# Kernel tuning notes

Hardware: AMD Instinct MI355X
Metric: run time of the kernel (lower is better)

The kernel has to match this reference:

```python
import jax, jax.numpy as jnp
import numpy as np

K = 1024
HEADS = 16


def setup_inputs() -> dict:
    key = jax.random.key(0)
    ks = jax.random.split(key, 6)
    x = jax.random.normal(ks[0], (2, 2048, K), dtype=jnp.float32)
    sc = 1.0 / np.sqrt(K)
    Wq = jax.random.normal(ks[1], (K, K), dtype=jnp.float32) * sc
    Wk = jax.random.normal(ks[2], (K, K), dtype=jnp.float32) * sc
    Wv = jax.random.normal(ks[3], (K, K), dtype=jnp.float32) * sc
    Wu = jax.random.normal(ks[4], (K, K), dtype=jnp.float32) * sc
    bu = jax.random.normal(ks[5], (K,), dtype=jnp.float32) * 0.01
    return {"x": x, "Wq": Wq, "Wk": Wk, "Wv": Wv, "Wu": Wu, "bu": bu}


def reference(x, Wq, Wk, Wv, Wu, bu):
    b, t, k = x.shape
    h = HEADS
    s = k // h
    # torch Linear: y = x @ W.T
    q = (x @ Wq.T).reshape(b, t, h, s)
    kk = (x @ Wk.T).reshape(b, t, h, s)
    v = (x @ Wv.T).reshape(b, t, h, s)
    # NOTE: original scales by sqrt(k) (full model dim), not sqrt(head dim)
    dot = jnp.einsum('bqhs,bkhs->bhqk', q, kk) / jnp.sqrt(jnp.float32(k))
    attn = jax.nn.softmax(dot, axis=-1)
    out = jnp.einsum('bhqk,bkhs->bqhs', attn, v).reshape(b, t, k)
    return out @ Wu.T + bu
```

## Files before the change

kernel.cpp:

```cpp
#include <hip/hip_runtime.h>
#include <hip/hip_bf16.h>


typedef __bf16 bf16x8 __attribute__((ext_vector_type(8)));
typedef float f32x4 __attribute__((ext_vector_type(4)));
typedef float f32x16 __attribute__((ext_vector_type(16)));
typedef unsigned int u32x4 __attribute__((ext_vector_type(4)));

static __device__ __forceinline__ unsigned short f2bf(float f) {
  union { float f; unsigned u; } a; a.f = f;
  unsigned r = a.u + 0x7fff + ((a.u >> 16) & 1);
  return (unsigned short)(r >> 16);
}

static __device__ __forceinline__ unsigned cvt_pk_bf16(float lo, float hi) {
  unsigned r;
  asm("v_cvt_pk_bf16_f32 %0, %1, %2" : "=v"(r) : "v"(lo), "v"(hi));
  return r;
}

static __device__ __forceinline__ float fexp2(float x) {
#if __has_builtin(__builtin_amdgcn_exp2f)
  return __builtin_amdgcn_exp2f(x);
#else
  float r; asm("v_exp_f32 %0, %1\n\ts_nop 0" : "=v"(r) : "v"(x)); return r;
#endif
}

static __device__ __forceinline__ void swap32(unsigned a, unsigned b,
                                              unsigned& x, unsigned& y, int hi) {
#if __has_builtin(__builtin_amdgcn_permlane32_swap)
  typedef unsigned u32x2 __attribute__((ext_vector_type(2)));
  u32x2 r = __builtin_amdgcn_permlane32_swap(a, b, false, false);
  x = r.x; y = r.y;
#else
  unsigned pa = (unsigned)__shfl_xor((int)a, 32, 64);
  unsigned pb = (unsigned)__shfl_xor((int)b, 32, 64);
  x = hi ? pb : a;
  y = hi ? b : pa;
#endif
}

static __device__ __forceinline__ void gload_lds16(const unsigned short* g, unsigned short* l) {
  __builtin_amdgcn_global_load_lds((const __attribute__((address_space(1))) void*)g,
                                   (__attribute__((address_space(3))) void*)l, 16, 0, 0);
}

static __device__ __forceinline__ float tsum16(const f32x16& v) {
  float a0 = v[0]+v[1], a1 = v[2]+v[3], a2 = v[4]+v[5], a3 = v[6]+v[7];
  float a4 = v[8]+v[9], a5 = v[10]+v[11], a6 = v[12]+v[13], a7 = v[14]+v[15];
  float b0 = a0+a1, b1 = a2+a3, b2 = a4+a5, b3 = a6+a7;
  return (b0+b1) + (b2+b3);
}

__global__ __launch_bounds__(256)
void cast_all(const float* __restrict__ x, const float* __restrict__ wq,
              const float* __restrict__ wk, const float* __restrict__ wv,
              const float* __restrict__ wu,
              unsigned short* __restrict__ xb, unsigned short* __restrict__ wqb,
              unsigned short* __restrict__ wkb, unsigned short* __restrict__ wvb,
              unsigned short* __restrict__ wub)
{
  int bid = blockIdx.x;
  const float* src; unsigned short* dst; int blk;
  if (bid < 4096)      { src = x;  dst = xb;  blk = bid; }
  else if (bid < 5120) { src = wq; dst = wqb; blk = bid - 4096; }
  else if (bid < 6144) { src = wk; dst = wkb; blk = bid - 5120; }
  else if (bid < 7168) { src = wv; dst = wvb; blk = bid - 6144; }
  else                 { src = wu; dst = wub; blk = bid - 7168; }
  int idx = blk * 1024 + threadIdx.x * 4;
  float4 v = *(const float4*)&src[idx];
  ushort4 o;
  o.x = f2bf(v.x); o.y = f2bf(v.y); o.z = f2bf(v.z); o.w = f2bf(v.w);
  *(ushort4*)&dst[idx] = o;
}

__global__ __launch_bounds__(512, 2)
void gemm_qkv(const unsigned short* __restrict__ A,
              const unsigned short* __restrict__ Bq,
              const unsigned short* __restrict__ Bk,
              const unsigned short* __restrict__ Bv,
              unsigned short* __restrict__ Qo,
              unsigned short* __restrict__ Ko,
              unsigned short* __restrict__ Vo)
{
  const int Ksz = 1024;
  __shared__ __align__(16) unsigned short As[2][128 * 64];
  __shared__ __align__(16) unsigned short Bs[2][128 * 64];
  const int z = blockIdx.z;
  const unsigned short* B = (z == 0) ? Bq : (z == 1) ? Bk : Bv;
  const int tid  = threadIdx.x;
  const int lane = tid & 63;
  const int wid  = tid >> 6;
  const int wr   = wid >> 2, wc = wid & 3;
  const int g    = lane >> 4, r = lane & 15;
  const int bm   = blockIdx.x * 128, bn = blockIdx.y * 128;

  f32x4 acc[4][2] = {};

  const int srow   = lane >> 3;
  const int schunk = (lane & 7) ^ srow;
  const unsigned short* Ag0 = &A[(size_t)(bm + wid*16 +     srow) * Ksz + schunk*8];
  const unsigned short* Ag1 = &A[(size_t)(bm + wid*16 + 8 + srow) * Ksz + schunk*8];
  const unsigned short* Bg0 = &B[(size_t)(bn + wid*16 +     srow) * Ksz + schunk*8];
  const unsigned short* Bg1 = &B[(size_t)(bn + wid*16 + 8 + srow) * Ksz + schunk*8];

  gload_lds16(Ag0, &As[0][(wid*16    ) * 64]);
  gload_lds16(Ag1, &As[0][(wid*16 + 8) * 64]);
  gload_lds16(Bg0, &Bs[0][(wid*16    ) * 64]);
  gload_lds16(Bg1, &Bs[0][(wid*16 + 8) * 64]);
  __syncthreads();

  int buf = 0;
  for (int k0 = 0; k0 < Ksz; k0 += 64) {
    if (k0 + 64 < Ksz) {
      gload_lds16(Ag0 + k0 + 64, &As[buf^1][(wid*16    ) * 64]);
      gload_lds16(Ag1 + k0 + 64, &As[buf^1][(wid*16 + 8) * 64]);
      gload_lds16(Bg0 + k0 + 64, &Bs[buf^1][(wid*16    ) * 64]);
      gload_lds16(Bg1 + k0 + 64, &Bs[buf^1][(wid*16 + 8) * 64]);
    }
#pragma unroll
    for (int kk = 0; kk < 2; ++kk) {
      bf16x8 af[4], bfr[2];
#pragma unroll
      for (int mi = 0; mi < 4; ++mi) {
        int row = wr*64 + mi*16 + r;
        int c = (g + kk*4) ^ (row & 7);
        af[mi] = *(const bf16x8*)&As[buf][row*64 + c*8];
      }
#pragma unroll
      for (int ni = 0; ni < 2; ++ni) {
        int row = wc*32 + ni*16 + r;
        int c = (g + kk*4) ^ (row & 7);
        bfr[ni] = *(const bf16x8*)&Bs[buf][row*64 + c*8];
      }
#pragma unroll
      for (int mi = 0; mi < 4; ++mi)
#pragma unroll
        for (int ni = 0; ni < 2; ++ni)
          acc[mi][ni] = __builtin_amdgcn_mfma_f32_16x16x32_bf16(af[mi], bfr[ni], acc[mi][ni], 0, 0, 0);
    }
    __syncthreads();
    buf ^= 1;
  }

  const float scale = (z == 0) ? (0.03125f * 1.4426950408889634f) : 1.0f;
#pragma unroll
  for (int mi = 0; mi < 4; ++mi)
#pragma unroll
    for (int ni = 0; ni < 2; ++ni) {
      if (z == 2) {
        int m0 = bm + wr*64 + mi*16 + g*4;
        int n  = bn + wc*32 + ni*16 + r;
        int b = m0 >> 11, t0 = m0 & 2047;
        int h = n >> 6,  s = n & 63;
        ushort4 o;
        o.x = f2bf(acc[mi][ni][0]); o.y = f2bf(acc[mi][ni][1]);
        o.z = f2bf(acc[mi][ni][2]); o.w = f2bf(acc[mi][ni][3]);
        *(ushort4*)&Vo[((size_t)((b*16 + h)*64 + s)) * 2048 + t0] = o;
      } else {
        unsigned short* dst = (z == 0) ? Qo : Ko;
#pragma unroll
        for (int q = 0; q < 4; ++q) {
          int m = bm + wr*64 + mi*16 + g*4 + q;
          int n = bn + wc*32 + ni*16 + r;
          int b = m >> 11, t = m & 2047;
          int h = n >> 6,  s = n & 63;
          dst[((size_t)((b*16 + h)*2048 + t)) * 64 + s] = f2bf(acc[mi][ni][q] * scale);
        }
      }
    }
}

__global__ __launch_bounds__(512, 2)
void gemm_final(const unsigned short* __restrict__ A,
                const unsigned short* __restrict__ B,
                float* __restrict__ Cf,
                const float* __restrict__ bias)
{
  const int Ksz = 1024, N = 1024;
  __shared__ __align__(16) unsigned short As[2][128 * 64];
  __shared__ __align__(16) unsigned short Bs[2][128 * 64];
  const int tid  = threadIdx.x;
  const int lane = tid & 63;
  const int wid  = tid >> 6;
  const int wr   = wid >> 2, wc = wid & 3;
  const int g    = lane >> 4, r = lane & 15;
  const int bm   = blockIdx.x * 128, bn = blockIdx.y * 128;

  f32x4 acc[4][2] = {};

  const int srow   = lane >> 3;
  const int schunk = (lane & 7) ^ srow;
  const unsigned short* Ag0 = &A[(size_t)(bm + wid*16 +     srow) * Ksz + schunk*8];
  const unsigned short* Ag1 = &A[(size_t)(bm + wid*16 + 8 + srow) * Ksz + schunk*8];
  const unsigned short* Bg0 = &B[(size_t)(bn + wid*16 +     srow) * Ksz + schunk*8];
  const unsigned short* Bg1 = &B[(size_t)(bn + wid*16 + 8 + srow) * Ksz + schunk*8];

  gload_lds16(Ag0, &As[0][(wid*16    ) * 64]);
  gload_lds16(Ag1, &As[0][(wid*16 + 8) * 64]);
  gload_lds16(Bg0, &Bs[0][(wid*16    ) * 64]);
  gload_lds16(Bg1, &Bs[0][(wid*16 + 8) * 64]);
  __syncthreads();

  int buf = 0;
  for (int k0 = 0; k0 < Ksz; k0 += 64) {
    if (k0 + 64 < Ksz) {
      gload_lds16(Ag0 + k0 + 64, &As[buf^1][(wid*16    ) * 64]);
      gload_lds16(Ag1 + k0 + 64, &As[buf^1][(wid*16 + 8) * 64]);
      gload_lds16(Bg0 + k0 + 64, &Bs[buf^1][(wid*16    ) * 64]);
      gload_lds16(Bg1 + k0 + 64, &Bs[buf^1][(wid*16 + 8) * 64]);
    }
#pragma unroll
    for (int kk = 0; kk < 2; ++kk) {
      bf16x8 af[4], bfr[2];
#pragma unroll
      for (int mi = 0; mi < 4; ++mi) {
        int row = wr*64 + mi*16 + r;
        int c = (g + kk*4) ^ (row & 7);
        af[mi] = *(const bf16x8*)&As[buf][row*64 + c*8];
      }
#pragma unroll
      for (int ni = 0; ni < 2; ++ni) {
        int row = wc*32 + ni*16 + r;
        int c = (g + kk*4) ^ (row & 7);
        bfr[ni] = *(const bf16x8*)&Bs[buf][row*64 + c*8];
      }
#pragma unroll
      for (int mi = 0; mi < 4; ++mi)
#pragma unroll
        for (int ni = 0; ni < 2; ++ni)
          acc[mi][ni] = __builtin_amdgcn_mfma_f32_16x16x32_bf16(af[mi], bfr[ni], acc[mi][ni], 0, 0, 0);
    }
    __syncthreads();
    buf ^= 1;
  }

#pragma unroll
  for (int mi = 0; mi < 4; ++mi)
#pragma unroll
    for (int ni = 0; ni < 2; ++ni)
#pragma unroll
      for (int q = 0; q < 4; ++q) {
        int m = bm + wr*64 + mi*16 + g*4 + q;
        int n = bn + wc*32 + ni*16 + r;
        Cf[(size_t)m * N + n] = acc[mi][ni][q] + bias[n];
      }
}

__global__ __launch_bounds__(256)
void attn_kernel(const unsigned short* __restrict__ Qg,
                 const unsigned short* __restrict__ Kg,
                 const unsigned short* __restrict__ Vtg,
                 unsigned short* __restrict__ Og)
{
  const int T = 2048;
  __shared__ __align__(16) unsigned short sK[2][128 * 64];
  __shared__ __align__(16) unsigned short sV[2][64 * 128];

  const int tid = threadIdx.x, lane = tid & 63, wid = tid >> 6;
  const int q32 = lane & 31;
  const int kh  = lane >> 5;

  int bid  = blockIdx.x + 16 * blockIdx.y;
  int nb   = (bid & 7) * 64 + (bid >> 3);
  int bh   = nb >> 4;
  int qblk = nb & 15;
  int qbase = qblk * 128 + wid * 32;

  const size_t base = (size_t)bh * T * 64;
  const unsigned short* Qh = Qg + base;
  const unsigned short* Kh = Kg + base;
  const unsigned short* Vh = Vtg + base;

  const int krow_l  = lane >> 3;
  const int kchunk  = (lane & 7) ^ (krow_l & 7);
  const int vrow_l  = lane >> 4;
  const int vchunkp = lane & 15;

  bf16x8 qf[4];
#pragma unroll
  for (int s = 0; s < 4; ++s)
    qf[s] = *(const bf16x8*)&Qh[(size_t)(qbase + q32)*64 + s*16 + kh*8];

  f32x16 oacc[2] = {};
  float l_own = 0.f;

#pragma unroll
  for (int r = 0; r < 4; ++r) {
    int kr = r*32 + wid*8;
    gload_lds16(Kh + (size_t)(kr + krow_l)*64 + kchunk*8, &sK[0][kr*64]);
    int vr = r*16 + wid*4;
    int vrow = vr + vrow_l;
    gload_lds16(Vh + (size_t)vrow*T + ((vchunkp ^ (vrow & 7))*8), &sV[0][vr*128]);
  }
  __syncthreads();

  int buf = 0;
#pragma unroll 1
  for (int t = 0; t < 16; ++t) {
    if (t < 15) {
      const int kv1 = (t + 1) * 128;
#pragma unroll
      for (int r = 0; r < 4; ++r) {
        int kr = r*32 + wid*8;
        gload_lds16(Kh + (size_t)(kv1 + kr + krow_l)*64 + kchunk*8,
                    &sK[buf^1][kr*64]);
        int vr = r*16 + wid*4;
        int vrow = vr + vrow_l;
        gload_lds16(Vh + (size_t)vrow*T + kv1 + ((vchunkp ^ (vrow & 7))*8),
                    &sV[buf^1][vr*128]);
      }
    }

#pragma unroll
    for (int st = 0; st < 4; ++st) {
      f32x16 a = {};
      const int kvr = st*32 + q32;
#pragma unroll
      for (int s = 0; s < 4; ++s) {
        const int c = (s*2 + kh) ^ (kvr & 7);
        bf16x8 kf = *(const bf16x8*)&sK[buf][kvr*64 + c*8];
        a = __builtin_amdgcn_mfma_f32_32x32x16_bf16(kf, qf[s], a, 0, 0, 0);
      }
#pragma unroll
      for (int r = 0; r < 16; ++r)
        a[r] = fexp2(a[r]);
      l_own += tsum16(a);

      unsigned U[8];
#pragma unroll
      for (int i = 0; i < 8; ++i)
        U[i] = cvt_pk_bf16(a[2*i], a[2*i + 1]);
      unsigned w[8];
      swap32(U[0], U[2], w[0], w[2], kh);
      swap32(U[1], U[3], w[1], w[3], kh);
      swap32(U[4], U[6], w[4], w[6], kh);
      swap32(U[5], U[7], w[5], w[7], kh);
#pragma unroll
      for (int c = 0; c < 2; ++c) {
        u32x4 pw = { w[c*4 + 0], w[c*4 + 1], w[c*4 + 2], w[c*4 + 3] };
        bf16x8 pf = __builtin_bit_cast(bf16x8, pw);
#pragma unroll
        for (int mt = 0; mt < 2; ++mt) {
          const int sr = mt*32 + q32;
          const int cc = (st*4 + c*2 + kh) ^ (sr & 7);
          bf16x8 vfr = *(const bf16x8*)&sV[buf][sr*128 + cc*8];
          oacc[mt] = __builtin_amdgcn_mfma_f32_32x32x16_bf16(vfr, pf, oacc[mt], 0, 0, 0);
        }
      }
    }

    __syncthreads();
    buf ^= 1;
  }

  const float l = l_own + __shfl_xor(l_own, 32, 64);
  const int h = bh & 15, b = bh >> 4;
  const float inv = 1.0f / l;
  const int tq = qbase + q32;
#pragma unroll
  for (int mt = 0; mt < 2; ++mt)
#pragma unroll
    for (int rg = 0; rg < 4; ++rg) {
      ushort4 o;
      o.x = f2bf(oacc[mt][rg*4 + 0] * inv);
      o.y = f2bf(oacc[mt][rg*4 + 1] * inv);
      o.z = f2bf(oacc[mt][rg*4 + 2] * inv);
      o.w = f2bf(oacc[mt][rg*4 + 3] * inv);
      int sd = mt*32 + rg*8 + kh*4;
      *(ushort4*)&Og[((size_t)(b*2048 + tq))*1024 + h*64 + sd] = o;
    }
}

extern "C" void kernel_launch(void* const* d_in, const int* in_sizes, int n_in,
                              void* d_out, int out_size, void* d_ws, size_t ws_size,
                              hipStream_t stream) {
  const float* x  = (const float*)d_in[0];
  const float* Wq = (const float*)d_in[1];
  const float* Wk = (const float*)d_in[2];
  const float* Wv = (const float*)d_in[3];
  const float* Wu = (const float*)d_in[4];
  const float* bu = (const float*)d_in[5];
  float* out = (float*)d_out;

  char* ws = (char*)d_ws;
  unsigned short* xb  = (unsigned short*)(ws);
  unsigned short* Wqb = (unsigned short*)(ws + (size_t)( 8<<20));
  unsigned short* Wkb = (unsigned short*)(ws + (size_t)(10<<20));
  unsigned short* Wvb = (unsigned short*)(ws + (size_t)(12<<20));
  unsigned short* Wub = (unsigned short*)(ws + (size_t)(14<<20));
  unsigned short* Qg  = (unsigned short*)(ws + (size_t)(16<<20));
  unsigned short* Kg  = (unsigned short*)(ws + (size_t)(24<<20));
  unsigned short* Vtg = (unsigned short*)(ws + (size_t)(32<<20));
  unsigned short* Ab  = xb;

  cast_all<<<dim3(8192), 256, 0, stream>>>(x, Wq, Wk, Wv, Wu, xb, Wqb, Wkb, Wvb, Wub);

  gemm_qkv<<<dim3(32, 8, 3), 512, 0, stream>>>(xb, Wqb, Wkb, Wvb, Qg, Kg, Vtg);

  attn_kernel<<<dim3(16, 32), 256, 0, stream>>>(Qg, Kg, Vtg, Ab);

  gemm_final<<<dim3(32, 8), 512, 0, stream>>>(Ab, Wub, out, bu);
}
```

Measured before the change: 114.9 us.

## Prefetch two tiles ahead with explicit vmcnt waits and raw barriers

Restructures the LDS double-buffer loops in the projection GEMMs and the attention kernel. Two tiles are staged up front, and each iteration refills the just-consumed buffer with the tile two steps ahead. Partial s_waitcnt vmcnt waits replace full __syncthreads so only the oldest loads must complete. This aims to keep more global loads in flight and hide memory latency. In exchange it adds a second barrier per iteration and relies on hand-counted vmcnt values being correct.

```diff
diff --git a/kernel.cpp b/kernel.cpp
--- a/kernel.cpp
+++ b/kernel.cpp
@@ -26,6 +26,10 @@
   float r; asm("v_exp_f32 %0, %1\n\ts_nop 0" : "=v"(r) : "v"(x)); return r;
 #endif
 }
+
+static __device__ __forceinline__ void wv8() { asm volatile("s_waitcnt vmcnt(8)" ::: "memory"); }
+static __device__ __forceinline__ void wv4() { asm volatile("s_waitcnt vmcnt(4)" ::: "memory"); }
+static __device__ __forceinline__ void wv0() { asm volatile("s_waitcnt vmcnt(0)" ::: "memory"); }
 
 static __device__ __forceinline__ void swap32(unsigned a, unsigned b,
                                               unsigned& x, unsigned& y, int hi) {
@@ -105,20 +109,21 @@
   const unsigned short* Bg0 = &B[(size_t)(bn + wid*16 +     srow) * Ksz + schunk*8];
   const unsigned short* Bg1 = &B[(size_t)(bn + wid*16 + 8 + srow) * Ksz + schunk*8];
 
-  gload_lds16(Ag0, &As[0][(wid*16    ) * 64]);
-  gload_lds16(Ag1, &As[0][(wid*16 + 8) * 64]);
-  gload_lds16(Bg0, &Bs[0][(wid*16    ) * 64]);
-  gload_lds16(Bg1, &Bs[0][(wid*16 + 8) * 64]);
-  __syncthreads();
-
-  int buf = 0;
-  for (int k0 = 0; k0 < Ksz; k0 += 64) {
-    if (k0 + 64 < Ksz) {
-      gload_lds16(Ag0 + k0 + 64, &As[buf^1][(wid*16    ) * 64]);
-      gload_lds16(Ag1 + k0 + 64, &As[buf^1][(wid*16 + 8) * 64]);
-      gload_lds16(Bg0 + k0 + 64, &Bs[buf^1][(wid*16    ) * 64]);
-      gload_lds16(Bg1 + k0 + 64, &Bs[buf^1][(wid*16 + 8) * 64]);
-    }
+  auto stage_step = [&](int kof, int b) {
+    gload_lds16(Ag0 + kof, &As[b][(wid*16    ) * 64]);
+    gload_lds16(Ag1 + kof, &As[b][(wid*16 + 8) * 64]);
+    gload_lds16(Bg0 + kof, &Bs[b][(wid*16    ) * 64]);
+    gload_lds16(Bg1 + kof, &Bs[b][(wid*16 + 8) * 64]);
+  };
+
+  stage_step(0,  0);
+  stage_step(64, 1);
+  wv4();
+  __builtin_amdgcn_s_barrier();
+
+#pragma unroll 1
+  for (int ks = 0; ks < 16; ++ks) {
+    const int buf = ks & 1;
 #pragma unroll
     for (int kk = 0; kk < 2; ++kk) {
       bf16x8 af[4], bfr[2];
@@ -140,8 +145,11 @@
         for (int ni = 0; ni < 2; ++ni)
           acc[mi][ni] = __builtin_amdgcn_mfma_f32_16x16x32_bf16(af[mi], bfr[ni], acc[mi][ni], 0, 0, 0);
     }
-    __syncthreads();
-    buf ^= 1;
+    if (ks == 15) break;
+    __builtin_amdgcn_s_barrier();
+    if (ks + 2 < 16) { stage_step((ks + 2) * 64, buf); wv4(); }
+    else             { wv0(); }
+    __builtin_amdgcn_s_barrier();
   }
 
   const float scale = (z == 0) ? (0.03125f * 1.4426950408889634f) : 1.0f;
@@ -197,20 +205,21 @@
   const unsigned short* Bg0 = &B[(size_t)(bn + wid*16 +     srow) * Ksz + schunk*8];
   const unsigned short* Bg1 = &B[(size_t)(bn + wid*16 + 8 + srow) * Ksz + schunk*8];
 
-  gload_lds16(Ag0, &As[0][(wid*16    ) * 64]);
-  gload_lds16(Ag1, &As[0][(wid*16 + 8) * 64]);
-  gload_lds16(Bg0, &Bs[0][(wid*16    ) * 64]);
-  gload_lds16(Bg1, &Bs[0][(wid*16 + 8) * 64]);
-  __syncthreads();
-
-  int buf = 0;
-  for (int k0 = 0; k0 < Ksz; k0 += 64) {
-    if (k0 + 64 < Ksz) {
-      gload_lds16(Ag0 + k0 + 64, &As[buf^1][(wid*16    ) * 64]);
-      gload_lds16(Ag1 + k0 + 64, &As[buf^1][(wid*16 + 8) * 64]);
-      gload_lds16(Bg0 + k0 + 64, &Bs[buf^1][(wid*16    ) * 64]);
-      gload_lds16(Bg1 + k0 + 64, &Bs[buf^1][(wid*16 + 8) * 64]);
-    }
+  auto stage_step = [&](int kof, int b) {
+    gload_lds16(Ag0 + kof, &As[b][(wid*16    ) * 64]);
+    gload_lds16(Ag1 + kof, &As[b][(wid*16 + 8) * 64]);
+    gload_lds16(Bg0 + kof, &Bs[b][(wid*16    ) * 64]);
+    gload_lds16(Bg1 + kof, &Bs[b][(wid*16 + 8) * 64]);
+  };
+
+  stage_step(0,  0);
+  stage_step(64, 1);
+  wv4();
+  __builtin_amdgcn_s_barrier();
+
+#pragma unroll 1
+  for (int ks = 0; ks < 16; ++ks) {
+    const int buf = ks & 1;
 #pragma unroll
     for (int kk = 0; kk < 2; ++kk) {
       bf16x8 af[4], bfr[2];
@@ -232,8 +241,11 @@
         for (int ni = 0; ni < 2; ++ni)
           acc[mi][ni] = __builtin_amdgcn_mfma_f32_16x16x32_bf16(af[mi], bfr[ni], acc[mi][ni], 0, 0, 0);
     }
-    __syncthreads();
-    buf ^= 1;
+    if (ks == 15) break;
+    __builtin_amdgcn_s_barrier();
+    if (ks + 2 < 16) { stage_step((ks + 2) * 64, buf); wv4(); }
+    else             { wv0(); }
+    __builtin_amdgcn_s_barrier();
   }
 
 #pragma unroll
@@ -278,6 +290,17 @@
   const int vrow_l  = lane >> 4;
   const int vchunkp = lane & 15;
 
+  auto stage_tile = [&](int kvb, int b) {
+#pragma unroll
+    for (int rr = 0; rr < 4; ++rr) {
+      int kr = rr*32 + wid*8;
+      gload_lds16(Kh + (size_t)(kvb + kr + krow_l)*64 + kchunk*8, &sK[b][kr*64]);
+      int vr = rr*16 + wid*4;
+      int vrow = vr + vrow_l;
+      gload_lds16(Vh + (size_t)vrow*T + kvb + ((vchunkp ^ (vrow & 7))*8), &sV[b][vr*128]);
+    }
+  };
+
   bf16x8 qf[4];
 #pragma unroll
   for (int s = 0; s < 4; ++s)
@@ -286,32 +309,14 @@
   f32x16 oacc[2] = {};
   float l_own = 0.f;
 
-#pragma unroll
-  for (int r = 0; r < 4; ++r) {
-    int kr = r*32 + wid*8;
-    gload_lds16(Kh + (size_t)(kr + krow_l)*64 + kchunk*8, &sK[0][kr*64]);
-    int vr = r*16 + wid*4;
-    int vrow = vr + vrow_l;
-    gload_lds16(Vh + (size_t)vrow*T + ((vchunkp ^ (vrow & 7))*8), &sV[0][vr*128]);
-  }
-  __syncthreads();
-
-  int buf = 0;
+  stage_tile(0,   0);
+  stage_tile(128, 1);
+  wv8();
+  __builtin_amdgcn_s_barrier();
+
 #pragma unroll 1
   for (int t = 0; t < 16; ++t) {
-    if (t < 15) {
-      const int kv1 = (t + 1) * 128;
-#pragma unroll
-      for (int r = 0; r < 4; ++r) {
-        int kr = r*32 + wid*8;
-        gload_lds16(Kh + (size_t)(kv1 + kr + krow_l)*64 + kchunk*8,
-                    &sK[buf^1][kr*64]);
-        int vr = r*16 + wid*4;
-        int vrow = vr + vrow_l;
-        gload_lds16(Vh + (size_t)vrow*T + kv1 + ((vchunkp ^ (vrow & 7))*8),
-                    &sV[buf^1][vr*128]);
-      }
-    }
+    const int buf = t & 1;
 
 #pragma unroll
     for (int st = 0; st < 4; ++st) {
@@ -324,8 +329,8 @@
         a = __builtin_amdgcn_mfma_f32_32x32x16_bf16(kf, qf[s], a, 0, 0, 0);
       }
 #pragma unroll
-      for (int r = 0; r < 16; ++r)
-        a[r] = fexp2(a[r]);
+      for (int rr = 0; rr < 16; ++rr)
+        a[rr] = fexp2(a[rr]);
       l_own += tsum16(a);
 
       unsigned U[8];
@@ -351,8 +356,11 @@
       }
     }
 
-    __syncthreads();
-    buf ^= 1;
+    if (t == 15) break;
+    __builtin_amdgcn_s_barrier();
+    if (t + 2 < 16) { stage_tile((t + 2) * 128, buf); wv8(); }
+    else            { wv0(); }
+    __builtin_amdgcn_s_barrier();
   }
 
   const float l = l_own + __shfl_xor(l_own, 32, 64);
```

Result: faster. 107.6 us, median of 3 (-6.3%).
